# Performance work log

Measured on AMD Instinct MI355X. Metric: run time of the kernel, lower is better.

The kernel has to match this reference:

```python
import jax, jax.numpy as jnp
import numpy as np

# Layer hyperparams (from TwoLayerSNN.__init__)
L1 = dict(thresh=0.5, tau_mem=10.0, tau_syn=5.0, dt=1.0, grad_type='gaussian', lens=0.5, gamma=1.0, hight=0.15)
L2 = dict(thresh=1.0, tau_mem=20.0, tau_syn=10.0, dt=1.0, grad_type='multi_gaussian', lens=0.4, gamma=1.2, hight=0.2)

B, T, D, H, O = 256, 1000, 32, 200, 2


def _gaussian(x, mu, sigma):
    return jnp.exp(-((x - mu) ** 2) / (2.0 * sigma ** 2)) / (jnp.sqrt(2.0 * jnp.pi) * sigma)


def make_spike(grad_type, lens, gamma, hight):
    """Heaviside forward, surrogate-gradient backward."""
    @jax.custom_vjp
    def spike(x):
        return (x > 0).astype(x.dtype)

    def fwd(x):
        return spike(x), x

    def bwd(x, g):
        if grad_type == 'gaussian':
            temp = _gaussian(x, 0.0, lens)
        else:  # multi_gaussian
            scale = 6.0
            temp = (_gaussian(x, 0.0, lens) * (1.0 + hight)
                    - _gaussian(x, lens, scale * lens) * hight
                    - _gaussian(x, -lens, scale * lens) * hight)
        return (g * temp * gamma,)

    spike.defvjp(fwd, bwd)
    return spike

_spike1 = make_spike(L1['grad_type'], L1['lens'], L1['gamma'], L1['hight'])
_spike2 = make_spike(L2['grad_type'], L2['lens'], L2['gamma'], L2['hight'])


def setup_inputs() -> dict:
    key = jax.random.key(0)
    k1, k2, k3 = jax.random.split(key, 3)
    x = jax.random.normal(k1, (B, T, D), dtype=jnp.float32)
    w1 = jax.random.normal(k2, (D, H), dtype=jnp.float32) / np.sqrt(D)
    w2 = jax.random.normal(k3, (H, O), dtype=jnp.float32) / np.sqrt(H)
    return {"x": x, "w1": w1, "w2": w2}


def _snn_forward(x, w1, w2):
    dtype = x.dtype
    # decay constants (compile-time scalars)
    a_syn1 = np.exp(-L1['dt'] / L1['tau_syn']); a_mem1 = np.exp(-L1['dt'] / L1['tau_mem'])
    in_sc1 = (1.0 - a_syn1) * L1['tau_syn']
    a_syn2 = np.exp(-L2['dt'] / L2['tau_syn']); a_mem2 = np.exp(-L2['dt'] / L2['tau_mem'])
    in_sc2 = (1.0 - a_syn2) * L2['tau_syn']
    th1, th2 = L1['thresh'], L2['thresh']

    b = x.shape[0]
    zeros = lambda n: jnp.zeros((b, n), dtype=dtype)
    init = (zeros(w1.shape[1]), zeros(w1.shape[1]), zeros(w2.shape[1]), zeros(w2.shape[1]))

    def step(carry, x_t):
        syn1, mem1, syn2, mem2 = carry
        syn1 = a_syn1 * syn1 + in_sc1 * (x_t @ w1)
        mem1 = a_mem1 * mem1 + (1.0 - a_mem1) * syn1
        s1 = _spike1(mem1 - th1)
        mem1 = mem1 - s1 * th1  # soft reset
        syn2 = a_syn2 * syn2 + in_sc2 * (s1 @ w2)
        mem2 = a_mem2 * mem2 + (1.0 - a_mem2) * syn2
        s2 = _spike2(mem2 - th2)
        mem2 = mem2 - s2 * th2  # soft reset
        return (syn1, mem1, syn2, mem2), (s1, mem1, s2, mem2)

    xt = jnp.swapaxes(x, 0, 1)  # [T, B, D]
    _, (s1, m1, s2, m2) = jax.lax.scan(step, init, xt)
    # accumulate post-reset mem2 for t>0, averaged over seq_length
    seq_len = x.shape[1]
    output = jnp.sum(m2[1:], axis=0) / seq_len  # [B, O]
    to_bt = lambda a: jnp.swapaxes(a, 0, 1)  # [B, T, ...]
    return output, to_bt(s1), to_bt(m1), to_bt(s2), to_bt(m2)


def reference(x, w1, w2):
    return _snn_forward(x, w1, w2)
```

## Files before the change

### kernel.cpp

```cpp
#include <hip/hip_runtime.h>


constexpr int TB = 256;
constexpr int TT = 1000;
constexpr int DD = 32;
constexpr int HH = 200;
constexpr int OO = 2;
constexpr int CH = 40;
constexpr int NCH = TT / CH;
constexpr int SC = 20;
constexpr int NSC = TT / SC;
constexpr int XF4 = CH * DD / 4;

typedef float v2f __attribute__((ext_vector_type(2)));

__device__ __forceinline__ v2f pk_fma(v2f a, v2f b, v2f c) {
#if __has_builtin(__builtin_elementwise_fma)
    return __builtin_elementwise_fma(a, b, c);
#else
    v2f r; r.x = fmaf(a.x, b.x, c.x); r.y = fmaf(a.y, b.y, c.y); return r;
#endif
}

template <int CTRL>
__device__ __forceinline__ float dpp_add(float v) {
    int t = __builtin_amdgcn_update_dpp(0, __float_as_int(v), CTRL, 0xf, 0xf, true);
    return v + __int_as_float(t);
}

__device__ __forceinline__ float read_lane_f(float v, int l) {
    return __int_as_float(__builtin_amdgcn_readlane(__float_as_int(v), l));
}

__device__ __forceinline__ void block_sync_lds() {
    asm volatile("s_waitcnt lgkmcnt(0)" ::: "memory");
    __builtin_amdgcn_s_barrier();
    asm volatile("" ::: "memory");
}

__global__ __launch_bounds__(576, 1)
void snn_fwd(const float* __restrict__ x,
             const float* __restrict__ w1,
             const float* __restrict__ w2,
             float* __restrict__ out)
{
    const int b    = blockIdx.x;
    const int tid  = threadIdx.x;
    const int lane = tid & 63;
    const int wid  = tid >> 6;
    const bool is_cons = (wid < 4);
    const bool is_prod = (wid >= 4 && wid < 8);
    const int ptid = tid - 256;
    const bool act = is_cons && (tid < HH);

    float* __restrict__ outp = out;
    float* __restrict__ s1o  = out + (size_t)TB * OO;
    float* __restrict__ m1o  = s1o + (size_t)TB * TT * HH;
    float* __restrict__ s2o  = m1o + (size_t)TB * TT * HH;
    float* __restrict__ m2o  = s2o + (size_t)TB * TT * OO;

    const float A_SYN1 = (float)0.8187307530779818;
    const float IN_SC1 = (float)((1.0 - 0.8187307530779818) * 5.0);
    const float A_MEM1 = (float)0.9048374180359595;
    const float B_MEM1 = (float)(1.0 - 0.9048374180359595);
    const float TH1    = 0.5f;
    const float A_SYN2 = (float)0.9048374180359595;
    const float IN_SC2 = (float)((1.0 - 0.9048374180359595) * 10.0);
    const float A_MEM2 = (float)0.9512294245007140;
    const float B_MEM2 = (float)(1.0 - 0.9512294245007140);
    const float TH2    = 1.0f;

    __shared__ float4 xls[2][XF4];
    __shared__ float  dotb[2][SC][HH];
    __shared__ __align__(16) float2 partv[2][SC][16];

    const float* __restrict__ xb = x + (size_t)b * TT * DD;

    const int ph   = (wid - 4) * 50 + lane;
    const bool pact = is_prod && (lane < 50);
    v2f w1e[DD / 4], w1o[DD / 4];
#pragma unroll
    for (int i = 0; i < DD / 4; ++i) {
        w1e[i] = pact ? v2f{w1[(4 * i) * HH + ph],     w1[(4 * i + 1) * HH + ph]} : v2f{0.f, 0.f};
        w1o[i] = pact ? v2f{w1[(4 * i + 2) * HH + ph], w1[(4 * i + 3) * HH + ph]} : v2f{0.f, 0.f};
    }
    const float w2x = act ? w2[tid * OO + 0] : 0.0f;
    const float w2y = act ? w2[tid * OO + 1] : 0.0f;

    if (is_cons) {
        const float4* g = (const float4*)xb;
        if (2 * tid     < XF4) xls[0][2 * tid]     = g[2 * tid];
        if (2 * tid + 1 < XF4) xls[0][2 * tid + 1] = g[2 * tid + 1];
    }
    block_sync_lds();

    auto produce = [&](int j) {
        const float4* xq = &xls[(j >> 1) & 1][(j & 1) * SC * (DD / 4)];
        float4 Xc0 = xq[0], Xc1 = xq[1], Xc2 = xq[2], Xc3 = xq[3];
        float4 Xc4 = xq[4], Xc5 = xq[5], Xc6 = xq[6], Xc7 = xq[7];
#pragma unroll
        for (int s = 0; s < SC; ++s) {
            float4 Xn0, Xn1, Xn2, Xn3, Xn4, Xn5, Xn6, Xn7;
            if (s < SC - 1) {
                const float4* nq = xq + (s + 1) * 8;
                Xn0 = nq[0]; Xn1 = nq[1]; Xn2 = nq[2]; Xn3 = nq[3];
                Xn4 = nq[4]; Xn5 = nq[5]; Xn6 = nq[6]; Xn7 = nq[7];
            }
            v2f A01 = {0.f, 0.f}, A23 = {0.f, 0.f};
            A01 = pk_fma(v2f{Xc0.x, Xc0.y}, w1e[0], A01);
            A23 = pk_fma(v2f{Xc0.z, Xc0.w}, w1o[0], A23);
            A01 = pk_fma(v2f{Xc1.x, Xc1.y}, w1e[1], A01);
            A23 = pk_fma(v2f{Xc1.z, Xc1.w}, w1o[1], A23);
            A01 = pk_fma(v2f{Xc2.x, Xc2.y}, w1e[2], A01);
            A23 = pk_fma(v2f{Xc2.z, Xc2.w}, w1o[2], A23);
            A01 = pk_fma(v2f{Xc3.x, Xc3.y}, w1e[3], A01);
            A23 = pk_fma(v2f{Xc3.z, Xc3.w}, w1o[3], A23);
            A01 = pk_fma(v2f{Xc4.x, Xc4.y}, w1e[4], A01);
            A23 = pk_fma(v2f{Xc4.z, Xc4.w}, w1o[4], A23);
            A01 = pk_fma(v2f{Xc5.x, Xc5.y}, w1e[5], A01);
            A23 = pk_fma(v2f{Xc5.z, Xc5.w}, w1o[5], A23);
            A01 = pk_fma(v2f{Xc6.x, Xc6.y}, w1e[6], A01);
            A23 = pk_fma(v2f{Xc6.z, Xc6.w}, w1o[6], A23);
            A01 = pk_fma(v2f{Xc7.x, Xc7.y}, w1e[7], A01);
            A23 = pk_fma(v2f{Xc7.z, Xc7.w}, w1o[7], A23);
            const float dotv = __fadd_rn(__fadd_rn(A01.x, A01.y),
                                         __fadd_rn(A23.x, A23.y));
            if (pact) dotb[j & 1][s][ph] = dotv;
            if (s < SC - 1) {
                Xc0 = Xn0; Xc1 = Xn1; Xc2 = Xn2; Xc3 = Xn3;
                Xc4 = Xn4; Xc5 = Xn5; Xc6 = Xn6; Xc7 = Xn7;
            }
        }
    };

    if (is_prod) produce(0);
    block_sync_lds();

    float syn1 = 0.0f, mem1 = 0.0f;
    double accx = 0.0, accy = 0.0;
    v2f syn2 = {0.f, 0.f}, mem2 = {0.f, 0.f};
    const v2f A2v  = {A_SYN2, A_SYN2};
    const v2f SC2v = {IN_SC2, IN_SC2};
    const v2f AM2v = {A_MEM2, A_MEM2};
    const v2f BM2v = {B_MEM2, B_MEM2};
    const v2f TH2v = {TH2, TH2};

    float* __restrict__ s1p = s1o + (size_t)b * TT * HH + tid;
    float* __restrict__ m1p = m1o + (size_t)b * TT * HH + tid;
    float2* __restrict__ s2p = (float2*)(s2o + (size_t)b * TT * OO);
    float2* __restrict__ m2p = (float2*)(m2o + (size_t)b * TT * OO);

    auto l2_chunk = [&](int j) {
#pragma clang fp contract(off)
        const int g = lane >> 4;
        const int p = lane & 15;
#pragma unroll
        for (int half = 0; half < SC / 4; ++half) {
            const float2 v = partv[j & 1][4 * half + g][p];
            float cxv = v.x, cyv = v.y;
            cxv = dpp_add<0x111>(cxv); cyv = dpp_add<0x111>(cyv);
            cxv = dpp_add<0x112>(cxv); cyv = dpp_add<0x112>(cyv);
            cxv = dpp_add<0x114>(cxv); cyv = dpp_add<0x114>(cyv);
            cxv = dpp_add<0x118>(cxv); cyv = dpp_add<0x118>(cyv);
#pragma unroll
            for (int gg = 0; gg < 4; ++gg) {
                const v2f d = {read_lane_f(cxv, 16 * gg + 15),
                               read_lane_f(cyv, 16 * gg + 15)};
                syn2 = (A2v * syn2) + (SC2v * d);
                mem2 = (AM2v * mem2) + (BM2v * syn2);
                const float s2x = (mem2.x - TH2 > 0.0f) ? 1.0f : 0.0f;
                const float s2y = (mem2.y - TH2 > 0.0f) ? 1.0f : 0.0f;
                const v2f s2v = {s2x, s2y};
                mem2 = mem2 - (s2v * TH2v);
                const int t = j * SC + 4 * half + gg;
                if (tid == 512) {
                    s2p[t] = make_float2(s2x, s2y);
                    m2p[t] = make_float2(mem2.x, mem2.y);
                }
                if (t > 0) { accx += (double)mem2.x; accy += (double)mem2.y; }
            }
        }
    };

    for (int sc = 0; sc < NSC; ++sc) {
        const int t0   = sc * SC;
        const int c    = t0 / CH;
        const int cpos = t0 % CH;

        if (is_cons) {
            float D[SC];
#pragma unroll
            for (int s = 0; s < SC; ++s) D[s] = dotb[sc & 1][s][tid];

#pragma unroll
            for (int s = 0; s < SC; ++s) {
                const float dot = D[s];
                syn1 = __fadd_rn(__fmul_rn(A_SYN1, syn1), __fmul_rn(IN_SC1, dot));
                mem1 = __fadd_rn(__fmul_rn(A_MEM1, mem1), __fmul_rn(B_MEM1, syn1));
                const float s1v = (mem1 - TH1 > 0.0f) ? 1.0f : 0.0f;
                mem1 = __fsub_rn(mem1, __fmul_rn(s1v, TH1));

                if (act) {
                    s1p[(size_t)(t0 + s) * HH] = s1v;
                    m1p[(size_t)(t0 + s) * HH] = mem1;
                }

                float cx = s1v * w2x;
                float cy = s1v * w2y;
                cx = dpp_add<0x111>(cx); cy = dpp_add<0x111>(cy);
                cx = dpp_add<0x112>(cx); cy = dpp_add<0x112>(cy);
                cx = dpp_add<0x114>(cx); cy = dpp_add<0x114>(cy);
                cx = dpp_add<0x118>(cx); cy = dpp_add<0x118>(cy);
                if ((lane & 15) == 15)
                    partv[sc & 1][s][wid * 4 + (lane >> 4)] = make_float2(cx, cy);
            }
        } else if (is_prod) {
            float4 pr0, pr1;
            const bool stage = (cpos == 0 && c + 1 < NCH);
            if (stage) {
                const float4* g = (const float4*)(xb + (size_t)(c + 1) * CH * DD);
                if (2 * ptid     < XF4) pr0 = g[2 * ptid];
                if (2 * ptid + 1 < XF4) pr1 = g[2 * ptid + 1];
            }

            if (sc + 1 < NSC) produce(sc + 1);

            if (stage) {
                if (2 * ptid     < XF4) xls[(c + 1) & 1][2 * ptid]     = pr0;
                if (2 * ptid + 1 < XF4) xls[(c + 1) & 1][2 * ptid + 1] = pr1;
            }
        } else {
            if (sc > 0) l2_chunk(sc - 1);
        }

        block_sync_lds();
    }

    if (wid == 8) {
        l2_chunk(NSC - 1);
        if (tid == 512) {
            outp[b * OO + 0] = (float)accx / 1000.0f;
            outp[b * OO + 1] = (float)accy / 1000.0f;
        }
    }
}

extern "C" void kernel_launch(void* const* d_in, const int* in_sizes, int n_in,
                              void* d_out, int out_size, void* d_ws, size_t ws_size,
                              hipStream_t stream) {
    const float* x  = (const float*)d_in[0];
    const float* w1 = (const float*)d_in[1];
    const float* w2 = (const float*)d_in[2];
    float* out = (float*)d_out;

    dim3 grid(TB), block(576);
    hipLaunchKernelGGL(snn_fwd, grid, block, 0, stream, x, w1, w2, out);
}
```

Baseline: 182.2 us.

## Offload layer-2 spike reduction to dedicated reducer waves in a deeper pipeline

Consumer waves no longer do the per-step DPP reduction of s1*w2. They write spikes to an LDS buffer instead. Four new reducer waves (block grows from 576 to 832 threads) compute the 200-wide dot products one stage later, and the layer-2 wave runs two stages behind. The aim is to shorten the serial layer-1 critical path on the consumer waves. The cost is extra LDS traffic, more waves per barrier, and a longer pipeline tail.

```diff
diff --git a/kernel.cpp b/kernel.cpp
--- a/kernel.cpp
+++ b/kernel.cpp
@@ -28,8 +28,13 @@
     return v + __int_as_float(t);
 }
 
-__device__ __forceinline__ float read_lane_f(float v, int l) {
-    return __int_as_float(__builtin_amdgcn_readlane(__float_as_int(v), l));
+__device__ __forceinline__ void wave_sum2(float& a, float& b) {
+    a = dpp_add<0x111>(a); b = dpp_add<0x111>(b);
+    a = dpp_add<0x112>(a); b = dpp_add<0x112>(b);
+    a = dpp_add<0x114>(a); b = dpp_add<0x114>(b);
+    a = dpp_add<0x118>(a); b = dpp_add<0x118>(b);
+    a = dpp_add<0x142>(a); b = dpp_add<0x142>(b);
+    a = dpp_add<0x143>(a); b = dpp_add<0x143>(b);
 }
 
 __device__ __forceinline__ void block_sync_lds() {
@@ -38,7 +43,7 @@
     asm volatile("" ::: "memory");
 }
 
-__global__ __launch_bounds__(576, 1)
+__global__ __launch_bounds__(832, 1)
 void snn_fwd(const float* __restrict__ x,
              const float* __restrict__ w1,
              const float* __restrict__ w2,
@@ -50,6 +55,8 @@
     const int wid  = tid >> 6;
     const bool is_cons = (wid < 4);
     const bool is_prod = (wid >= 4 && wid < 8);
+    const bool is_red  = (wid >= 8 && wid < 12);
+    const bool is_l2   = (wid == 12);
     const int ptid = tid - 256;
     const bool act = is_cons && (tid < HH);
 
@@ -72,7 +79,8 @@
 
     __shared__ float4 xls[2][XF4];
     __shared__ float  dotb[2][SC][HH];
-    __shared__ __align__(16) float2 partv[2][SC][16];
+    __shared__ float  s1ls[2][SC][HH];
+    __shared__ __align__(8) float2 partq[2][SC];
 
     const float* __restrict__ xb = x + (size_t)b * TT * DD;
 
@@ -84,8 +92,14 @@
         w1e[i] = pact ? v2f{w1[(4 * i) * HH + ph],     w1[(4 * i + 1) * HH + ph]} : v2f{0.f, 0.f};
         w1o[i] = pact ? v2f{w1[(4 * i + 2) * HH + ph], w1[(4 * i + 3) * HH + ph]} : v2f{0.f, 0.f};
     }
-    const float w2x = act ? w2[tid * OO + 0] : 0.0f;
-    const float w2y = act ? w2[tid * OO + 1] : 0.0f;
+    float w2xa[4], w2ya[4];
+#pragma unroll
+    for (int k = 0; k < 4; ++k) {
+        const int h = lane + 64 * k;
+        const bool v = is_red && (h < HH);
+        w2xa[k] = v ? w2[h * OO + 0] : 0.0f;
+        w2ya[k] = v ? w2[h * OO + 1] : 0.0f;
+    }
 
     if (is_cons) {
         const float4* g = (const float4*)xb;
@@ -150,35 +164,45 @@
     float2* __restrict__ s2p = (float2*)(s2o + (size_t)b * TT * OO);
     float2* __restrict__ m2p = (float2*)(m2o + (size_t)b * TT * OO);
 
+    auto reduce_chunk = [&](int j) {
+        const int rw = wid - 8;
+#pragma unroll
+        for (int q = 0; q < 5; ++q) {
+            const int s = rw * 5 + q;
+            const float* sp = &s1ls[j & 1][s][0];
+            float cx = 0.0f, cy = 0.0f;
+#pragma unroll
+            for (int k = 0; k < 4; ++k) {
+                const int h = lane + 64 * k;
+                const float sv = (h < HH) ? sp[h] : 0.0f;
+                cx = fmaf(sv, w2xa[k], cx);
+                cy = fmaf(sv, w2ya[k], cy);
+            }
+            wave_sum2(cx, cy);
+            if (lane == 63) partq[j & 1][s] = make_float2(cx, cy);
+        }
+    };
+
     auto l2_chunk = [&](int j) {
 #pragma clang fp contract(off)
-        const int g = lane >> 4;
-        const int p = lane & 15;
-#pragma unroll
-        for (int half = 0; half < SC / 4; ++half) {
-            const float2 v = partv[j & 1][4 * half + g][p];
-            float cxv = v.x, cyv = v.y;
-            cxv = dpp_add<0x111>(cxv); cyv = dpp_add<0x111>(cyv);
-            cxv = dpp_add<0x112>(cxv); cyv = dpp_add<0x112>(cyv);
-            cxv = dpp_add<0x114>(cxv); cyv = dpp_add<0x114>(cyv);
-            cxv = dpp_add<0x118>(cxv); cyv = dpp_add<0x118>(cyv);
-#pragma unroll
-            for (int gg = 0; gg < 4; ++gg) {
-                const v2f d = {read_lane_f(cxv, 16 * gg + 15),
-                               read_lane_f(cyv, 16 * gg + 15)};
-                syn2 = (A2v * syn2) + (SC2v * d);
-                mem2 = (AM2v * mem2) + (BM2v * syn2);
-                const float s2x = (mem2.x - TH2 > 0.0f) ? 1.0f : 0.0f;
-                const float s2y = (mem2.y - TH2 > 0.0f) ? 1.0f : 0.0f;
-                const v2f s2v = {s2x, s2y};
-                mem2 = mem2 - (s2v * TH2v);
-                const int t = j * SC + 4 * half + gg;
-                if (tid == 512) {
-                    s2p[t] = make_float2(s2x, s2y);
-                    m2p[t] = make_float2(mem2.x, mem2.y);
-                }
-                if (t > 0) { accx += (double)mem2.x; accy += (double)mem2.y; }
-            }
+        float2 P[SC];
+#pragma unroll
+        for (int s = 0; s < SC; ++s) P[s] = partq[j & 1][s];
+#pragma unroll
+        for (int s = 0; s < SC; ++s) {
+            const v2f d = {P[s].x, P[s].y};
+            syn2 = (A2v * syn2) + (SC2v * d);
+            mem2 = (AM2v * mem2) + (BM2v * syn2);
+            const float s2x = (mem2.x - TH2 > 0.0f) ? 1.0f : 0.0f;
+            const float s2y = (mem2.y - TH2 > 0.0f) ? 1.0f : 0.0f;
+            const v2f s2v = {s2x, s2y};
+            mem2 = mem2 - (s2v * TH2v);
+            const int t = j * SC + s;
+            if (tid == 768) {
+                s2p[t] = make_float2(s2x, s2y);
+                m2p[t] = make_float2(mem2.x, mem2.y);
+            }
+            if (t > 0) { accx += (double)mem2.x; accy += (double)mem2.y; }
         }
     };
 
@@ -203,16 +227,8 @@
                 if (act) {
                     s1p[(size_t)(t0 + s) * HH] = s1v;
                     m1p[(size_t)(t0 + s) * HH] = mem1;
+                    s1ls[sc & 1][s][tid] = s1v;
                 }
-
-                float cx = s1v * w2x;
-                float cy = s1v * w2y;
-                cx = dpp_add<0x111>(cx); cy = dpp_add<0x111>(cy);
-                cx = dpp_add<0x112>(cx); cy = dpp_add<0x112>(cy);
-                cx = dpp_add<0x114>(cx); cy = dpp_add<0x114>(cy);
-                cx = dpp_add<0x118>(cx); cy = dpp_add<0x118>(cy);
-                if ((lane & 15) == 15)
-                    partv[sc & 1][s][wid * 4 + (lane >> 4)] = make_float2(cx, cy);
             }
         } else if (is_prod) {
             float4 pr0, pr1;
@@ -229,16 +245,21 @@
                 if (2 * ptid     < XF4) xls[(c + 1) & 1][2 * ptid]     = pr0;
                 if (2 * ptid + 1 < XF4) xls[(c + 1) & 1][2 * ptid + 1] = pr1;
             }
+        } else if (is_red) {
+            if (sc > 0) reduce_chunk(sc - 1);
         } else {
-            if (sc > 0) l2_chunk(sc - 1);
+            if (sc > 1) l2_chunk(sc - 2);
         }
 
         block_sync_lds();
     }
 
-    if (wid == 8) {
+    if (is_red) reduce_chunk(NSC - 1);
+    if (is_l2)  l2_chunk(NSC - 2);
+    block_sync_lds();
+    if (is_l2) {
         l2_chunk(NSC - 1);
-        if (tid == 512) {
+        if (tid == 768) {
             outp[b * OO + 0] = (float)accx / 1000.0f;
             outp[b * OO + 1] = (float)accy / 1000.0f;
         }
@@ -253,6 +274,6 @@
     const float* w2 = (const float*)d_in[2];
     float* out = (float*)d_out;
 
-    dim3 grid(TB), block(576);
+    dim3 grid(TB), block(832);
     hipLaunchKernelGGL(snn_fwd, grid, block, 0, stream, x, w1, w2, out);
 }
```

After: 218.7 us. 20.0% more time.
